# Performance work log

Hardware: AMD Instinct MI355X
Metric: run time of the kernel (lower is better)

## Reference

```python
import jax, jax.numpy as jnp
from jax import lax
import numpy as np

B, QLEN, HQ, HKV, D, MAXLEN = 16, 1, 32, 8, 128, 8192
END_INDEX = 4096


def setup_inputs() -> dict:
    key = jax.random.key(0)
    k1, k2, k3, k4, k5 = jax.random.split(key, 5)
    query = jax.random.normal(k1, (B, QLEN, HQ, D), dtype=jnp.float32)
    new_key = jax.random.normal(k2, (B, QLEN, HKV, D), dtype=jnp.float32)
    new_value = jax.random.normal(k3, (B, QLEN, HKV, D), dtype=jnp.float32)
    key_cache = jax.random.normal(k4, (B, MAXLEN, HKV, D), dtype=jnp.float32)
    value_cache = jax.random.normal(k5, (B, MAXLEN, HKV, D), dtype=jnp.float32)
    attention_mask = jnp.ones((B, MAXLEN), dtype=jnp.bool_)
    # standard lower-triangular causal mask, (1, 1, L, L)
    causal_mask = jnp.tril(jnp.ones((MAXLEN, MAXLEN), dtype=jnp.bool_))[None, None]
    return {
        "query": query,
        "key": new_key,
        "value": new_value,
        "key_cache": key_cache,
        "value_cache": value_cache,
        "attention_mask": attention_mask,
        "causal_mask": causal_mask,
        "end_index": END_INDEX,
    }


def reference(query, key, value, key_cache, value_cache, attention_mask, causal_mask, end_index):
    # Faithful translation of FlaxAttentionModule._concatenate_to_cache + bias
    # construction in `concatenate` (decode path with a cache_view).
    num_updated = query.shape[1]              # q_len
    max_length = value_cache.shape[1]
    dtype = query.dtype

    # attention_mask: (B, L) -> (B, 1, 1, L)
    mask = attention_mask[:, None, None, :]

    # causal mask slice at the current write position: (1,1,q_len,L)
    cm = lax.dynamic_slice(causal_mask, (0, 0, end_index, 0), (1, 1, num_updated, max_length))
    cm = jnp.broadcast_to(cm, (query.shape[0],) + cm.shape[1:])
    mask = jnp.logical_and(jnp.broadcast_to(mask, cm.shape), cm)

    # scatter the new key/value into the ring-buffer cache
    slice_indices = (0, end_index % max_length, 0, 0)
    value_cache = lax.dynamic_update_slice(value_cache, value, slice_indices)
    key_cache = lax.dynamic_update_slice(key_cache, key, slice_indices)

    # pad mask: positions beyond the filled prefix are invalid
    pad_mask = jnp.broadcast_to(
        jnp.arange(max_length) < end_index + num_updated,
        (query.shape[0], 1, num_updated, max_length),
    )
    mask = jnp.logical_and(pad_mask, mask)

    # attention bias: 0 where attended, finfo.min where masked
    attention_bias = jnp.where(
        mask,
        jnp.zeros((), dtype),
        jnp.full((), jnp.finfo(dtype).min, dtype),
    )
    return key_cache, value_cache, mask, attention_bias
```

## Files before the change

### kernel.cpp

```cpp
#include <hip/hip_runtime.h>

#define BATCH   16
#define MAXLEN  8192
#define HKV     8
#define HDIM    128
#define ROWF    (HKV * HDIM)
#define ROW4    (ROWF / 4)
#define CACHE_F (BATCH * MAXLEN * ROWF)
#define CACHE_4 (CACHE_F / 4)
#define NMASK   (BATCH * MAXLEN)
#define TOTAL4  (2 * CACHE_4)

typedef float v4f __attribute__((ext_vector_type(4)));

__global__ __launch_bounds__(256) void fused_copy_fixup_mask(
    const v4f* __restrict__ key_cache,
    const v4f* __restrict__ value_cache,
    const v4f* __restrict__ new_key,
    const v4f* __restrict__ new_value,
    const unsigned char* __restrict__ attn_mask,
    const unsigned char* __restrict__ causal_mask,
    const int* __restrict__ end_index_p,
    v4f* __restrict__ out4,
    float* __restrict__ mask_out,
    float* __restrict__ bias_out)
{
    const int tid      = blockIdx.x * blockDim.x + threadIdx.x;
    const int nthreads = gridDim.x * blockDim.x;
    const int end      = *end_index_p;
    const int upd_s    = end & (MAXLEN - 1);

    if (tid < NMASK / 4) {
        const int j0 = (tid * 4) & (MAXLEN - 1);
        const uchar4 am = *(const uchar4*)(attn_mask + tid * 4);
        const uchar4 cm = *(const uchar4*)(causal_mask
                              + (long long)end * MAXLEN + j0);
        const float neg_big = __uint_as_float(0xFF7F0000u);
        const unsigned char amv[4] = {am.x, am.y, am.z, am.w};
        const unsigned char cmv[4] = {cm.x, cm.y, cm.z, cm.w};
        v4f m, bs;
        #pragma unroll
        for (int k = 0; k < 4; ++k) {
            const bool mm = amv[k] && cmv[k] && ((j0 + k) < (end + 1));
            m[k]  = mm ? 1.0f : 0.0f;
            bs[k] = mm ? 0.0f : neg_big;
        }
        *(v4f*)(mask_out + tid * 4) = m;
        *(v4f*)(bias_out + tid * 4) = bs;
    }

    for (int idx = tid; idx < TOTAL4; idx += nthreads) {
        const int half   = idx >> 25;
        const int within = idx & (CACHE_4 - 1);
        const int row    = within >> 8;
        const int s      = row & (MAXLEN - 1);
        v4f val;
        if (s == upd_s) {
            const int b = row >> 13;
            const int r = within & (ROW4 - 1);
            val = (half ? new_value : new_key)[b * ROW4 + r];
        } else {
            val = __builtin_nontemporal_load(
                (half ? value_cache : key_cache) + within);
        }
        __builtin_nontemporal_store(val, out4 + idx);
    }
}

extern "C" void kernel_launch(void* const* d_in, const int* in_sizes, int n_in,
                              void* d_out, int out_size, void* d_ws, size_t ws_size,
                              hipStream_t stream) {
    const v4f* new_key     = (const v4f*)d_in[1];
    const v4f* new_value   = (const v4f*)d_in[2];
    const v4f* key_cache   = (const v4f*)d_in[3];
    const v4f* value_cache = (const v4f*)d_in[4];
    const unsigned char* attn_mask   = (const unsigned char*)d_in[5];
    const unsigned char* causal_mask = (const unsigned char*)d_in[6];
    const int* end_index_p = (const int*)d_in[7];

    float* out      = (float*)d_out;
    float* mask_out = out + 2LL * CACHE_F;
    float* bias_out = mask_out + NMASK;

    fused_copy_fixup_mask<<<2048, 256, 0, stream>>>(
        key_cache, value_cache, new_key, new_value,
        attn_mask, causal_mask, end_index_p,
        (v4f*)d_out, mask_out, bias_out);
}
```

Baseline: 440.7 us.

## Tile cache copy per block with batched loads and post-copy row fixup

Replaces the grid-stride per-element copy loop with a tiled scheme: each block copies a contiguous 128-row tile of one cache, issuing eight independent 16-byte loads before eight stores. The per-element branch that checked for the updated row is gone; the block whose tile holds that row overwrites it with the new key or value after the bulk copy. Nontemporal load/store hints are dropped in favor of plain accesses. The goal is more memory-level parallelism and less per-element index math and divergence, at the cost of higher register pressure and a redundant write of one row.

```diff
diff --git a/kernel.cpp b/kernel.cpp
--- a/kernel.cpp
+++ b/kernel.cpp
@@ -10,6 +10,10 @@
 #define CACHE_4 (CACHE_F / 4)
 #define NMASK   (BATCH * MAXLEN)
 #define TOTAL4  (2 * CACHE_4)
+
+#define TILE4   32768
+#define TROWS   128
+#define NTILES  (TOTAL4 / TILE4)
 
 typedef float v4f __attribute__((ext_vector_type(4)));
 
@@ -25,11 +29,12 @@
     float* __restrict__ mask_out,
     float* __restrict__ bias_out)
 {
-    const int tid      = blockIdx.x * blockDim.x + threadIdx.x;
-    const int nthreads = gridDim.x * blockDim.x;
-    const int end      = *end_index_p;
-    const int upd_s    = end & (MAXLEN - 1);
+    const int t   = threadIdx.x;
+    const int blk = blockIdx.x;
+    const int end   = *end_index_p;
+    const int upd_s = end & (MAXLEN - 1);
 
+    const int tid = blk * 256 + t;
     if (tid < NMASK / 4) {
         const int j0 = (tid * 4) & (MAXLEN - 1);
         const uchar4 am = *(const uchar4*)(attn_mask + tid * 4);
@@ -49,21 +54,40 @@
         *(v4f*)(bias_out + tid * 4) = bs;
     }
 
-    for (int idx = tid; idx < TOTAL4; idx += nthreads) {
-        const int half   = idx >> 25;
-        const int within = idx & (CACHE_4 - 1);
-        const int row    = within >> 8;
-        const int s      = row & (MAXLEN - 1);
-        v4f val;
-        if (s == upd_s) {
-            const int b = row >> 13;
-            const int r = within & (ROW4 - 1);
-            val = (half ? new_value : new_key)[b * ROW4 + r];
-        } else {
-            val = __builtin_nontemporal_load(
-                (half ? value_cache : key_cache) + within);
-        }
-        __builtin_nontemporal_store(val, out4 + idx);
+    const int half          = blk >> 10;
+    const int tile_in_cache = blk & 1023;
+    const int b             = tile_in_cache >> 6;
+    const int s0            = (tile_in_cache & 63) * TROWS;
+
+    const v4f* __restrict__ src =
+        (half ? value_cache : key_cache)
+        + (long long)tile_in_cache * TILE4 + t;
+    v4f* __restrict__ dst = out4 + (long long)blk * TILE4 + t;
+
+    #pragma unroll
+    for (int jj = 0; jj < TROWS; jj += 8) {
+        v4f v0 = src[(jj + 0) * ROW4];
+        v4f v1 = src[(jj + 1) * ROW4];
+        v4f v2 = src[(jj + 2) * ROW4];
+        v4f v3 = src[(jj + 3) * ROW4];
+        v4f v4 = src[(jj + 4) * ROW4];
+        v4f v5 = src[(jj + 5) * ROW4];
+        v4f v6 = src[(jj + 6) * ROW4];
+        v4f v7 = src[(jj + 7) * ROW4];
+        dst[(jj + 0) * ROW4] = v0;
+        dst[(jj + 1) * ROW4] = v1;
+        dst[(jj + 2) * ROW4] = v2;
+        dst[(jj + 3) * ROW4] = v3;
+        dst[(jj + 4) * ROW4] = v4;
+        dst[(jj + 5) * ROW4] = v5;
+        dst[(jj + 6) * ROW4] = v6;
+        dst[(jj + 7) * ROW4] = v7;
+    }
+
+    const int fj = upd_s - s0;
+    if (fj >= 0 && fj < TROWS) {
+        const v4f* __restrict__ nsrc = half ? new_value : new_key;
+        dst[fj * ROW4] = nsrc[b * ROW4 + t];
     }
 }
 
@@ -82,7 +106,7 @@
     float* mask_out = out + 2LL * CACHE_F;
     float* bias_out = mask_out + NMASK;
 
-    fused_copy_fixup_mask<<<2048, 256, 0, stream>>>(
+    fused_copy_fixup_mask<<<NTILES, 256, 0, stream>>>(
         key_cache, value_cache, new_key, new_value,
         attn_mask, causal_mask, end_index_p,
         (v4f*)d_out, mask_out, bias_out);
```

After: 404.5 us. 8.2% less time.

## Split cache copy into unconditional K/V stream plus post-copy row fixup

Applied to the files above, without the earlier changes.

Replaces the per-element branch on the updated row with a branch-free unrolled loop that copies key and value caches together, then has the threads owning the updated row overwrite it with the new key/value after their own copy. This removes per-iteration index math and divergence and issues two independent loads per iteration for more memory-level parallelism. It drops the nontemporal load/store hints and writes the updated row twice. Correctness relies on the same thread performing both the bulk copy and the fixup for the slot, and on ITERS dividing evenly, since the grid size is now hard-coded.

```diff
diff --git a/kernel.cpp b/kernel.cpp
--- a/kernel.cpp
+++ b/kernel.cpp
@@ -9,7 +9,10 @@
 #define CACHE_F (BATCH * MAXLEN * ROWF)
 #define CACHE_4 (CACHE_F / 4)
 #define NMASK   (BATCH * MAXLEN)
-#define TOTAL4  (2 * CACHE_4)
+
+#define NBLOCKS  2048
+#define NTHREADS (NBLOCKS * 256)
+#define ITERS    (CACHE_4 / NTHREADS)
 
 typedef float v4f __attribute__((ext_vector_type(4)));
 
@@ -25,10 +28,9 @@
     float* __restrict__ mask_out,
     float* __restrict__ bias_out)
 {
-    const int tid      = blockIdx.x * blockDim.x + threadIdx.x;
-    const int nthreads = gridDim.x * blockDim.x;
-    const int end      = *end_index_p;
-    const int upd_s    = end & (MAXLEN - 1);
+    const int tid   = blockIdx.x * 256 + threadIdx.x;
+    const int end   = *end_index_p;
+    const int upd_s = end & (MAXLEN - 1);
 
     if (tid < NMASK / 4) {
         const int j0 = (tid * 4) & (MAXLEN - 1);
@@ -49,21 +51,27 @@
         *(v4f*)(bias_out + tid * 4) = bs;
     }
 
-    for (int idx = tid; idx < TOTAL4; idx += nthreads) {
-        const int half   = idx >> 25;
-        const int within = idx & (CACHE_4 - 1);
-        const int row    = within >> 8;
-        const int s      = row & (MAXLEN - 1);
-        v4f val;
-        if (s == upd_s) {
-            const int b = row >> 13;
-            const int r = within & (ROW4 - 1);
-            val = (half ? new_value : new_key)[b * ROW4 + r];
-        } else {
-            val = __builtin_nontemporal_load(
-                (half ? value_cache : key_cache) + within);
+    const v4f* __restrict__ kc = key_cache   + tid;
+    const v4f* __restrict__ vc = value_cache + tid;
+    v4f* __restrict__ ok = out4 + tid;
+    v4f* __restrict__ ov = out4 + CACHE_4 + tid;
+    #pragma unroll 8
+    for (int it = 0; it < ITERS; ++it) {
+        const int off = it * NTHREADS;
+        v4f a = kc[off];
+        v4f b = vc[off];
+        ok[off] = a;
+        ov[off] = b;
+    }
+
+    const int r = tid - ((upd_s & 2047) << 8);
+    if (r >= 0 && r < ROW4) {
+        #pragma unroll
+        for (int b = 0; b < BATCH; ++b) {
+            const long long o = ((long long)b * MAXLEN + upd_s) * ROW4 + r;
+            out4[o]           = new_key[b * ROW4 + r];
+            out4[CACHE_4 + o] = new_value[b * ROW4 + r];
         }
-        __builtin_nontemporal_store(val, out4 + idx);
     }
 }
 
@@ -82,7 +90,7 @@
     float* mask_out = out + 2LL * CACHE_F;
     float* bias_out = mask_out + NMASK;
 
-    fused_copy_fixup_mask<<<2048, 256, 0, stream>>>(
+    fused_copy_fixup_mask<<<NBLOCKS, 256, 0, stream>>>(
         key_cache, value_cache, new_key, new_value,
         attn_mask, causal_mask, end_index_p,
         (v4f*)d_out, mask_out, bias_out);
```

Result: slower. 517.0 us (+17.3%).
